# Optimization experiments

Hardware: AMD Instinct MI355X
Metric: run time of the kernel (lower is better)

The kernel has to match this reference:

```python
import jax, jax.numpy as jnp
import numpy as np

N_NODES = 50000
N_GRAPHS = 64
HEADS = 4
OUT_CH = 32
HC = HEADS * OUT_CH  # 128
F_IN = 32
EDGE_DIM = 1
NEG_SLOPE = 0.2


def gat_conv(x, edge_index, W, att_src, att_dst, bias, edge_attr=None, W_edge=None, att_edge=None):
    """PyG GATConv (concat=True, add_self_loops=True, fill_value='mean', eval mode)."""
    N = x.shape[0]
    H, C = att_src.shape
    xs = (x @ W).reshape(N, H, C)                      # [N,H,C]
    a_src = (xs * att_src).sum(-1)                     # [N,H]
    a_dst = (xs * att_dst).sum(-1)                     # [N,H]

    src, dst = edge_index[0], edge_index[1]
    loops = jnp.arange(N)
    src_sl = jnp.concatenate([src, loops])
    dst_sl = jnp.concatenate([dst, loops])

    alpha = a_src[src_sl] + a_dst[dst_sl]              # [E+N,H]
    if edge_attr is not None:
        # self-loop edge_attr = per-dst mean of incoming edge_attr (fill_value='mean')
        cnt = jax.ops.segment_sum(jnp.ones_like(dst, dtype=edge_attr.dtype), dst, N)
        loop_attr = jax.ops.segment_sum(edge_attr, dst, N) / jnp.maximum(cnt, 1.0)[:, None]
        ea = jnp.concatenate([edge_attr, loop_attr], axis=0)
        e = (ea @ W_edge).reshape(-1, H, C)
        alpha = alpha + (e * att_edge).sum(-1)

    alpha = jax.nn.leaky_relu(alpha, NEG_SLOPE)
    # segment softmax over incoming edges of each dst node
    amax = jax.ops.segment_max(alpha, dst_sl, N)       # every node has a self loop
    alpha = jnp.exp(alpha - amax[dst_sl])
    denom = jax.ops.segment_sum(alpha, dst_sl, N)
    alpha = alpha / (denom[dst_sl] + 1e-16)

    msg = xs[src_sl] * alpha[:, :, None]               # [E+N,H,C]
    out = jax.ops.segment_sum(msg, dst_sl, N)          # [N,H,C]
    return out.reshape(N, H * C) + bias


def setup_inputs() -> dict:
    key = jax.random.key(0)
    ks = iter(jax.random.split(key, 40))
    d = {}
    d["x"] = jax.random.normal(next(ks), (N_NODES, F_IN), jnp.float32)
    d["covalent_index"] = jax.random.randint(next(ks), (2, 150000), 0, N_NODES)
    d["distance_index"] = jax.random.randint(next(ks), (2, 1600000), 0, N_NODES)
    d["distance_attr"] = jax.random.uniform(next(ks), (1600000, EDGE_DIM), jnp.float32)
    d["batch"] = jnp.sort(jax.random.randint(next(ks), (N_NODES,), 0, N_GRAPHS))

    def p(shape):
        return jax.random.normal(next(ks), shape, jnp.float32) * 0.1

    for name, fin in [("c1", F_IN), ("c2", HC), ("d1", F_IN), ("d2", HC)]:
        d[f"W_{name}"] = p((fin, HC))
        d[f"as_{name}"] = p((HEADS, OUT_CH))
        d[f"ad_{name}"] = p((HEADS, OUT_CH))
        d[f"b_{name}"] = p((HC,))
    for name in ("d1", "d2"):
        d[f"We_{name}"] = p((EDGE_DIM, HC))
        d[f"ae_{name}"] = p((HEADS, OUT_CH))
    d["ff_W"] = p((HC, 128))
    d["ff_b"] = p((128,))
    d["out_W"] = p((128, 1))
    d["out_b"] = p((1,))
    return d


def reference(x, covalent_index, distance_index, distance_attr, batch,
              W_c1, as_c1, ad_c1, b_c1, W_c2, as_c2, ad_c2, b_c2,
              W_d1, as_d1, ad_d1, b_d1, We_d1, ae_d1,
              W_d2, as_d2, ad_d2, b_d2, We_d2, ae_d2,
              ff_W, ff_b, out_W, out_b):
    # covalent branch
    x1 = gat_conv(x, covalent_index, W_c1, as_c1, ad_c1, b_c1)
    x1 = jax.nn.relu(x1)
    x1 = gat_conv(x1, covalent_index, W_c2, as_c2, ad_c2, b_c2)
    # distance branch (with edge attributes)
    x2 = gat_conv(x, distance_index, W_d1, as_d1, ad_d1, b_d1, distance_attr, We_d1, ae_d1)
    x2 = jax.nn.relu(x2)
    x2 = gat_conv(x2, distance_index, W_d2, as_d2, ad_d2, b_d2, distance_attr, We_d2, ae_d2)
    h = (x1 + x2) * 0.5
    # global mean pool per graph
    sums = jax.ops.segment_sum(h, batch, N_GRAPHS)
    cnts = jax.ops.segment_sum(jnp.ones((h.shape[0],), h.dtype), batch, N_GRAPHS)
    g = sums / jnp.maximum(cnts, 1.0)[:, None]
    g = jax.nn.relu(g @ ff_W + ff_b)
    # dropout(p=0.3) treated as identity (eval / deterministic reference)
    return jax.nn.sigmoid(g @ out_W + out_b)
```

## Files before the change

### kernel.cpp

```cpp
#include <hip/hip_runtime.h>
#include <math.h>

#define NEG_SLOPE 0.2f

__device__ __forceinline__ float lrelu(float x){ return x > 0.f ? x : NEG_SLOPE * x; }
__device__ __forceinline__ float bf_lo(unsigned u){ return __uint_as_float(u << 16); }
__device__ __forceinline__ float bf_hi(unsigned u){ return __uint_as_float(u & 0xffff0000u); }
__device__ __forceinline__ unsigned short f2bf(float v){
  unsigned ub = __float_as_uint(v);
  return (unsigned short)((ub + 0x7FFFu + ((ub >> 16) & 1u)) >> 16);
}

template<int K>
__global__ __launch_bounds__(256) void transform2_kernel(
    const float* __restrict__ A, const float* __restrict__ W,
    const float* __restrict__ att_s, const float* __restrict__ att_d,
    unsigned short* __restrict__ xs, float* __restrict__ a_src,
    float* __restrict__ a_dst, int N){
  constexpr int KC = (K < 32) ? K : 32;
  __shared__ float sW[KC][128];
  __shared__ float sA[32][K];
  const int tid = threadIdx.x;
  const int j4  = (tid & 31) * 4;
  const int ng  = tid >> 5;
  const int h   = (tid & 31) >> 3;

  const float4 as = *reinterpret_cast<const float4*>(att_s + j4);
  const float4 ad = *reinterpret_cast<const float4*>(att_d + j4);

  const int ntiles = (N + 31) >> 5;
  for (int tile = blockIdx.x; tile < ntiles; tile += gridDim.x){
    const int n0 = tile << 5;
    for (int idx = tid; idx < 32 * K; idx += 256){
      int nn = idx / K, kk = idx - nn * K;
      int node = n0 + nn;
      sA[nn][kk] = (node < N) ? A[(size_t)node * K + kk] : 0.f;
    }

    float acc[4][4];
    #pragma unroll
    for (int m = 0; m < 4; ++m)
      #pragma unroll
      for (int e = 0; e < 4; ++e) acc[m][e] = 0.f;

    for (int kc0 = 0; kc0 < K; kc0 += KC){
      __syncthreads();
      for (int idx = tid; idx < KC * 128; idx += 256)
        sW[idx >> 7][idx & 127] = W[(size_t)(kc0 + (idx >> 7)) * 128 + (idx & 127)];
      __syncthreads();
      #pragma unroll 4
      for (int k = 0; k < KC; ++k){
        const float4 w = *reinterpret_cast<const float4*>(&sW[k][j4]);
        #pragma unroll
        for (int m = 0; m < 4; ++m){
          const float a = sA[ng * 4 + m][kc0 + k];
          acc[m][0] += a * w.x; acc[m][1] += a * w.y;
          acc[m][2] += a * w.z; acc[m][3] += a * w.w;
        }
      }
    }

    #pragma unroll
    for (int m = 0; m < 4; ++m){
      const int node = n0 + ng * 4 + m;
      const bool ok = node < N;
      if (ok){
        uint2 pk;
        pk.x = (unsigned)f2bf(acc[m][0]) | ((unsigned)f2bf(acc[m][1]) << 16);
        pk.y = (unsigned)f2bf(acc[m][2]) | ((unsigned)f2bf(acc[m][3]) << 16);
        *reinterpret_cast<uint2*>(xs + (size_t)node * 128 + j4) = pk;
      }
      float ss = acc[m][0]*as.x + acc[m][1]*as.y + acc[m][2]*as.z + acc[m][3]*as.w;
      float sd = acc[m][0]*ad.x + acc[m][1]*ad.y + acc[m][2]*ad.z + acc[m][3]*ad.w;
      #pragma unroll
      for (int d = 1; d < 8; d <<= 1){ ss += __shfl_xor(ss, d); sd += __shfl_xor(sd, d); }
      if (ok && (tid & 7) == 0){
        a_src[node * 4 + h] = ss;
        a_dst[node * 4 + h] = sd;
      }
    }
    __syncthreads();
  }
}

__global__ void count_kernel(const int* __restrict__ ei, int E, int* __restrict__ cnt){
  int e = blockIdx.x * blockDim.x + threadIdx.x;
  if (e < E) atomicAdd(&cnt[ei[E + e]], 1);
}

__global__ void blocksum_kernel(const int* __restrict__ cnt, int N, int* __restrict__ bsum){
  const int base = blockIdx.x * 1024;
  int s = 0;
  for (int i = threadIdx.x; i < 1024; i += 256){
    int idx = base + i;
    if (idx < N) s += cnt[idx];
  }
  #pragma unroll
  for (int d = 1; d < 64; d <<= 1) s += __shfl_xor(s, d);
  __shared__ int ws[4];
  if ((threadIdx.x & 63) == 0) ws[threadIdx.x >> 6] = s;
  __syncthreads();
  if (threadIdx.x == 0) bsum[blockIdx.x] = ws[0] + ws[1] + ws[2] + ws[3];
}

__global__ void bscan_kernel(int* __restrict__ bsum, int nb){
  int t = threadIdx.x;
  int v = (t < nb) ? bsum[t] : 0;
  int x = v;
  #pragma unroll
  for (int d = 1; d < 64; d <<= 1){ int y = __shfl_up(x, d); if (t >= d) x += y; }
  if (t < nb) bsum[t] = x - v;
}

__global__ void scanwrite_kernel(const int* __restrict__ cnt, const int* __restrict__ bsum,
                                 int N, int* __restrict__ rp, int* __restrict__ cur){
  const int b = blockIdx.x, t = threadIdx.x;
  const int base = b * 1024 + t * 4;
  int v0=0,v1=0,v2=0,v3=0;
  if (base + 0 < N) v0 = cnt[base + 0];
  if (base + 1 < N) v1 = cnt[base + 1];
  if (base + 2 < N) v2 = cnt[base + 2];
  if (base + 3 < N) v3 = cnt[base + 3];
  const int tsum = v0 + v1 + v2 + v3;
  int x = tsum;
  const int lane = t & 63;
  #pragma unroll
  for (int d = 1; d < 64; d <<= 1){ int y = __shfl_up(x, d); if (lane >= d) x += y; }
  __shared__ int ws[4];
  if (lane == 63) ws[t >> 6] = x;
  __syncthreads();
  int ofs = bsum[b];
  for (int w = 0; w < (t >> 6); ++w) ofs += ws[w];
  int start = ofs + (x - tsum);
  int r1 = start + v0, r2 = r1 + v1, r3 = r2 + v2, r4 = r3 + v3;
  if (base + 0 < N){ rp[base + 1] = r1; cur[base + 0] = start; }
  if (base + 1 < N){ rp[base + 2] = r2; cur[base + 1] = r1; }
  if (base + 2 < N){ rp[base + 3] = r3; cur[base + 2] = r2; }
  if (base + 3 < N){ rp[base + 4] = r4; cur[base + 3] = r3; }
  if (b == 0 && t == 0) rp[0] = 0;
}

__global__ void fill_cov_kernel(const int* __restrict__ ei, int E,
                                int* __restrict__ cur, int* __restrict__ csrc){
  int e = blockIdx.x * blockDim.x + threadIdx.x;
  if (e >= E) return;
  int src = ei[e];
  int dst = ei[E + e];
  int pos = atomicAdd(&cur[dst], 1);
  csrc[pos] = src;
}

__global__ void fill_dist_kernel(const int* __restrict__ ei, const float* __restrict__ eattr,
                                 int E, int* __restrict__ cur, int2* __restrict__ pke){
  int e = blockIdx.x * blockDim.x + threadIdx.x;
  if (e >= E) return;
  int src = ei[e];
  int dst = ei[E + e];
  float ea = eattr[e];
  int pos = atomicAdd(&cur[dst], 1);
  pke[pos] = make_int2(src, __float_as_int(ea));
}

__global__ void loopea_kernel(const int* __restrict__ rp, const int2* __restrict__ pke,
                              float* __restrict__ lea, int N){
  int n = blockIdx.x * blockDim.x + threadIdx.x;
  if (n >= N) return;
  int b = rp[n], e = rp[n+1];
  float s = 0.f;
  for (int i = b; i < e; ++i) s += __int_as_float(pke[i].y);
  lea[n] = s / fmaxf((float)(e - b), 1.f);
}

__global__ void coef_kernel(const float* __restrict__ We1, const float* __restrict__ ae1,
                            const float* __restrict__ We2, const float* __restrict__ ae2,
                            float* __restrict__ coef){
  int t = threadIdx.x;
  if (t < 4){
    float s = 0.f;
    for (int c = 0; c < 32; ++c) s += We1[t*32 + c] * ae1[t*32 + c];
    coef[t] = s;
  } else if (t < 8){
    int h = t - 4;
    float s = 0.f;
    for (int c = 0; c < 32; ++c) s += We2[h*32 + c] * ae2[h*32 + c];
    coef[4 + h] = s;
  }
}

template<bool HASE, bool RELU>
__global__ void gat_kernel(const int* __restrict__ rp, const int* __restrict__ csrc,
                           const int2* __restrict__ pke, const float* __restrict__ loopea,
                           const float* __restrict__ coef,
                           const unsigned short* __restrict__ xs, const float* __restrict__ a_src,
                           const float* __restrict__ a_dst, const float* __restrict__ bias,
                           float* __restrict__ out, int N){
  const int wv = threadIdx.x >> 6;
  const int lane = threadIdx.x & 63;
  const int n = blockIdx.x * 4 + wv;
  if (n >= N) return;

  const int beg = rp[n], end = rp[n+1];
  const int c = lane * 2;
  const int h = lane >> 4;

  const float adh = a_dst[(size_t)n*4 + h];
  const float ch  = HASE ? coef[h] : 0.f;

  float p;
  {
    float lea = HASE ? loopea[n] : 0.f;
    p = __expf(lrelu(a_src[(size_t)n*4 + h] + adh + lea * ch));
  }
  float denom = p;
  unsigned us = *reinterpret_cast<const unsigned*>(xs + (size_t)n*128 + c);
  float accx = p * bf_lo(us);
  float accy = p * bf_hi(us);

  #pragma unroll 4
  for (int i = beg; i < end; ++i){
    int s;
    float al;
    if (HASE){
      int2 pk = pke[i];
      s = pk.x;
      al = a_src[(size_t)s*4 + h] + adh + __int_as_float(pk.y) * ch;
    } else {
      s = csrc[i];
      al = a_src[(size_t)s*4 + h] + adh;
    }
    float pe = __expf(lrelu(al));
    denom += pe;
    unsigned u = *reinterpret_cast<const unsigned*>(xs + (size_t)s*128 + c);
    accx += pe * bf_lo(u);
    accy += pe * bf_hi(u);
  }

  const float inv = 1.f / (denom + 1e-16f);
  float ox = accx * inv + bias[c];
  float oy = accy * inv + bias[c+1];
  if (RELU){ ox = fmaxf(ox, 0.f); oy = fmaxf(oy, 0.f); }
  out[(size_t)n*128 + c]     = ox;
  out[(size_t)n*128 + c + 1] = oy;
}

template<bool COUNT>
__global__ void pool_kernel(const float* __restrict__ a, const int* __restrict__ batch,
                            float* __restrict__ sums, int* __restrict__ cnts, int N){
  const int j = threadIdx.x;
  const int n0 = blockIdx.x * 32;
  const int n1 = min(n0 + 32, N);
  if (n0 >= N) return;
  int g = batch[n0];
  float acc = 0.f;
  int cnt = 0;
  for (int n = n0; n < n1; ++n){
    int gn = batch[n];
    if (gn != g){
      atomicAdd(&sums[g*128 + j], 0.5f * acc);
      if (COUNT && j == 0) atomicAdd(&cnts[g], cnt);
      acc = 0.f; cnt = 0; g = gn;
    }
    acc += a[(size_t)n*128 + j];
    ++cnt;
  }
  atomicAdd(&sums[g*128 + j], 0.5f * acc);
  if (COUNT && j == 0) atomicAdd(&cnts[g], cnt);
}

__global__ void head_kernel(const float* __restrict__ sums, const int* __restrict__ cnts,
                            const float* __restrict__ ffW, const float* __restrict__ ffb,
                            const float* __restrict__ outW, const float* __restrict__ outb,
                            float* __restrict__ out){
  int g = blockIdx.x, j = threadIdx.x;
  __shared__ float mean[128];
  __shared__ float red[128];
  float cnt = fmaxf((float)cnts[g], 1.f);
  mean[j] = sums[g*128 + j] / cnt;
  __syncthreads();
  float acc = ffb[j];
  #pragma unroll 8
  for (int k = 0; k < 128; ++k) acc += mean[k] * ffW[k*128 + j];
  acc = fmaxf(acc, 0.f);
  red[j] = acc * outW[j];
  __syncthreads();
  for (int s = 64; s > 0; s >>= 1){
    if (j < s) red[j] += red[j + s];
    __syncthreads();
  }
  if (j == 0) out[g] = 1.f / (1.f + expf(-(red[0] + outb[0])));
}

extern "C" void kernel_launch(void* const* d_in, const int* in_sizes, int n_in,
                              void* d_out, int out_size, void* d_ws, size_t ws_size,
                              hipStream_t stream) {
  const float* x     = (const float*)d_in[0];
  const int*   cov   = (const int*)d_in[1];
  const int*   dist  = (const int*)d_in[2];
  const float* dattr = (const float*)d_in[3];
  const int*   batch = (const int*)d_in[4];
  const float* W_c1 = (const float*)d_in[5],  *as_c1 = (const float*)d_in[6],
             *ad_c1 = (const float*)d_in[7],  *b_c1  = (const float*)d_in[8];
  const float* W_c2 = (const float*)d_in[9],  *as_c2 = (const float*)d_in[10],
             *ad_c2 = (const float*)d_in[11], *b_c2  = (const float*)d_in[12];
  const float* W_d1 = (const float*)d_in[13], *as_d1 = (const float*)d_in[14],
             *ad_d1 = (const float*)d_in[15], *b_d1  = (const float*)d_in[16];
  const float* W_d2 = (const float*)d_in[17], *as_d2 = (const float*)d_in[18],
             *ad_d2 = (const float*)d_in[19], *b_d2  = (const float*)d_in[20];
  const float* We_d1 = (const float*)d_in[21], *ae_d1 = (const float*)d_in[22];
  const float* We_d2 = (const float*)d_in[23], *ae_d2 = (const float*)d_in[24];
  const float* ffW = (const float*)d_in[25], *ffb = (const float*)d_in[26];
  const float* outW = (const float*)d_in[27], *outb = (const float*)d_in[28];
  float* out = (float*)d_out;

  const int N  = in_sizes[0] / 32;
  const int Ec = in_sizes[1] / 2;
  const int Ed = in_sizes[2] / 2;

  char* p = (char*)d_ws;
  auto alloc = [&](size_t bytes) -> void* {
    void* r = (void*)p;
    p += (bytes + 255) & ~(size_t)255;
    return r;
  };
  float*          act    = (float*)alloc((size_t)N * 128 * 4);
  unsigned short* xs     = (unsigned short*)alloc((size_t)N * 128 * 2);
  float*          a_s    = (float*)alloc((size_t)N * 4 * 4);
  float*          a_d    = (float*)alloc((size_t)N * 4 * 4);
  int*            rp_c   = (int*)alloc((size_t)(N + 1) * 4);
  int*            rp_d   = (int*)alloc((size_t)(N + 1) * 4);
  int*            csrc_c = (int*)alloc((size_t)Ec * 4);
  int2*           pke_d  = (int2*)alloc((size_t)Ed * 8);
  int*            cnt    = (int*)alloc((size_t)N * 4);
  int*            cur    = (int*)alloc((size_t)N * 4);
  float*          lea    = (float*)alloc((size_t)N * 4);
  float*          coef   = (float*)alloc(8 * 4);
  float*          sums   = (float*)alloc(64 * 128 * 4);
  int*            cnts   = (int*)alloc(64 * 4);
  int*            bsum   = (int*)alloc(256 * 4);

  const int TB = 256;
  const int nb = (N + 1023) / 1024;
  hipMemsetAsync(cnt, 0, (size_t)N * 4, stream);
  count_kernel<<<(Ec + TB - 1) / TB, TB, 0, stream>>>(cov, Ec, cnt);
  blocksum_kernel<<<nb, 256, 0, stream>>>(cnt, N, bsum);
  bscan_kernel<<<1, 64, 0, stream>>>(bsum, nb);
  scanwrite_kernel<<<nb, 256, 0, stream>>>(cnt, bsum, N, rp_c, cur);
  fill_cov_kernel<<<(Ec + TB - 1) / TB, TB, 0, stream>>>(cov, Ec, cur, csrc_c);
  hipMemsetAsync(cnt, 0, (size_t)N * 4, stream);
  count_kernel<<<(Ed + TB - 1) / TB, TB, 0, stream>>>(dist, Ed, cnt);
  blocksum_kernel<<<nb, 256, 0, stream>>>(cnt, N, bsum);
  bscan_kernel<<<1, 64, 0, stream>>>(bsum, nb);
  scanwrite_kernel<<<nb, 256, 0, stream>>>(cnt, bsum, N, rp_d, cur);
  fill_dist_kernel<<<(Ed + TB - 1) / TB, TB, 0, stream>>>(dist, dattr, Ed, cur, pke_d);
  loopea_kernel<<<(N + TB - 1) / TB, TB, 0, stream>>>(rp_d, pke_d, lea, N);
  coef_kernel<<<1, 64, 0, stream>>>(We_d1, ae_d1, We_d2, ae_d2, coef);

  hipMemsetAsync(sums, 0, 64 * 128 * 4, stream);
  hipMemsetAsync(cnts, 0, 64 * 4, stream);

  const int gatGrid  = (N + 3) / 4;
  const int poolGrid = (N + 31) / 32;
  const int TFB = 1024;
  transform2_kernel<32><<<TFB, 256, 0, stream>>>(x, W_c1, as_c1, ad_c1, xs, a_s, a_d, N);
  gat_kernel<false, true><<<gatGrid, 256, 0, stream>>>(rp_c, csrc_c, nullptr, nullptr, nullptr,
                                                       xs, a_s, a_d, b_c1, act, N);
  transform2_kernel<128><<<TFB, 256, 0, stream>>>(act, W_c2, as_c2, ad_c2, xs, a_s, a_d, N);
  gat_kernel<false, false><<<gatGrid, 256, 0, stream>>>(rp_c, csrc_c, nullptr, nullptr, nullptr,
                                                        xs, a_s, a_d, b_c2, act, N);
  pool_kernel<true><<<poolGrid, 128, 0, stream>>>(act, batch, sums, cnts, N);
  transform2_kernel<32><<<TFB, 256, 0, stream>>>(x, W_d1, as_d1, ad_d1, xs, a_s, a_d, N);
  gat_kernel<true, true><<<gatGrid, 256, 0, stream>>>(rp_d, nullptr, pke_d, lea, coef,
                                                      xs, a_s, a_d, b_d1, act, N);
  transform2_kernel<128><<<TFB, 256, 0, stream>>>(act, W_d2, as_d2, ad_d2, xs, a_s, a_d, N);
  gat_kernel<true, false><<<gatGrid, 256, 0, stream>>>(rp_d, nullptr, pke_d, lea, coef + 4,
                                                       xs, a_s, a_d, b_d2, act, N);
  pool_kernel<false><<<poolGrid, 128, 0, stream>>>(act, batch, sums, nullptr, N);
  head_kernel<<<64, 128, 0, stream>>>(sums, cnts, ffW, ffb, outW, outb, out);
}
```

Measured before the change: 698.7 us.

## Precompute edge attention weights cooperatively per wavefront via shared memory

The GAT aggregation loop now handles incoming edges in chunks of 64. Each lane loads one edge's source index and edge attribute, computes the four per-head attention exponentials with one float4 a_src load, and stores them in LDS. The whole wavefront then walks the chunk, reading the source index and weight from LDS and gathering features. This removes the redundant per-lane index loads, a_src gathers and exp computations that the old serial loop repeated across all 64 lanes. The cost is LDS traffic and a wavefront-level dependency between the write and read phases, with no explicit barrier (it relies on wavefront lockstep).

```diff
diff --git a/kernel.cpp b/kernel.cpp
--- a/kernel.cpp
+++ b/kernel.cpp
@@ -194,6 +194,8 @@
                            const unsigned short* __restrict__ xs, const float* __restrict__ a_src,
                            const float* __restrict__ a_dst, const float* __restrict__ bias,
                            float* __restrict__ out, int N){
+  __shared__ float p_sh[4][64][4];
+  __shared__ int   s_sh[4][64];
   const int wv = threadIdx.x >> 6;
   const int lane = threadIdx.x & 63;
   const int n = blockIdx.x * 4 + wv;
@@ -203,36 +205,50 @@
   const int c = lane * 2;
   const int h = lane >> 4;
 
-  const float adh = a_dst[(size_t)n*4 + h];
-  const float ch  = HASE ? coef[h] : 0.f;
+  const float4 adv = *reinterpret_cast<const float4*>(a_dst + (size_t)n*4);
+  float4 cf = make_float4(0.f,0.f,0.f,0.f);
+  if (HASE) cf = *reinterpret_cast<const float4*>(coef);
+  const float adh = (h==0)?adv.x:(h==1)?adv.y:(h==2)?adv.z:adv.w;
+  const float chh = (h==0)?cf.x:(h==1)?cf.y:(h==2)?cf.z:cf.w;
 
   float p;
   {
     float lea = HASE ? loopea[n] : 0.f;
-    p = __expf(lrelu(a_src[(size_t)n*4 + h] + adh + lea * ch));
+    p = __expf(lrelu(a_src[(size_t)n*4 + h] + adh + lea * chh));
   }
   float denom = p;
   unsigned us = *reinterpret_cast<const unsigned*>(xs + (size_t)n*128 + c);
   float accx = p * bf_lo(us);
   float accy = p * bf_hi(us);
 
-  #pragma unroll 4
-  for (int i = beg; i < end; ++i){
-    int s;
-    float al;
-    if (HASE){
-      int2 pk = pke[i];
-      s = pk.x;
-      al = a_src[(size_t)s*4 + h] + adh + __int_as_float(pk.y) * ch;
-    } else {
-      s = csrc[i];
-      al = a_src[(size_t)s*4 + h] + adh;
-    }
-    float pe = __expf(lrelu(al));
-    denom += pe;
-    unsigned u = *reinterpret_cast<const unsigned*>(xs + (size_t)s*128 + c);
-    accx += pe * bf_lo(u);
-    accy += pe * bf_hi(u);
+  for (int c0 = beg; c0 < end; c0 += 64){
+    const int cnt = min(64, end - c0);
+    if (lane < cnt){
+      int s; float ea = 0.f;
+      if (HASE){
+        int2 rec = pke[c0 + lane];
+        s = rec.x; ea = __int_as_float(rec.y);
+      } else {
+        s = csrc[c0 + lane];
+      }
+      const float4 av = *reinterpret_cast<const float4*>(a_src + (size_t)s*4);
+      float4 pv;
+      pv.x = __expf(lrelu(av.x + adv.x + ea*cf.x));
+      pv.y = __expf(lrelu(av.y + adv.y + ea*cf.y));
+      pv.z = __expf(lrelu(av.z + adv.z + ea*cf.z));
+      pv.w = __expf(lrelu(av.w + adv.w + ea*cf.w));
+      *reinterpret_cast<float4*>(&p_sh[wv][lane][0]) = pv;
+      s_sh[wv][lane] = s;
+    }
+    #pragma unroll 4
+    for (int i = 0; i < cnt; ++i){
+      const int s = s_sh[wv][i];
+      const float pf = p_sh[wv][i][h];
+      denom += pf;
+      unsigned u = *reinterpret_cast<const unsigned*>(xs + (size_t)s*128 + c);
+      accx += pf * bf_lo(u);
+      accy += pf * bf_hi(u);
+    }
   }
 
   const float inv = 1.f / (denom + 1e-16f);
```

Result: faster. 673.5 us (-3.6%).
